# Kernel tuning notes

Hardware: AMD Instinct MI355X
Metric: run time of the kernel (lower is better)

## Reference

```python
import jax, jax.numpy as jnp
import numpy as np

B, T, D_IN, H, C = 4096, 20, 300, 512, 10


def setup_inputs() -> dict:
    key = jax.random.key(0)
    ks = jax.random.split(key, 12)
    s = lambda fan_in, fan_out: float(np.sqrt(6.0 / (fan_in + fan_out)))  # xavier uniform bound
    u = lambda k, shape, b: jax.random.uniform(k, shape, jnp.float32, -b, b)
    return {
        "x": jax.random.normal(ks[0], (B, T, D_IN), jnp.float32),
        "W_emb": u(ks[1], (D_IN, H), s(D_IN, H)),
        "b_emb": jnp.zeros((H,), jnp.float32),
        "wx0": u(ks[2], (H, H), s(H, H)),
        "wh0": u(ks[3], (H, H), s(H, H)),
        "b0": jnp.zeros((H,), jnp.float32),
        "wx1": u(ks[4], (H, H), s(H, H)),
        "wh1": u(ks[5], (H, H), s(H, H)),
        "b1": jnp.zeros((H,), jnp.float32),
        "wx2": u(ks[6], (H, H), s(H, H)),
        "wh2": u(ks[7], (H, H), s(H, H)),
        "b2": jnp.zeros((H,), jnp.float32),
        "W_fc": u(ks[8], (H, C), s(H, C)),
        "b_fc": jnp.zeros((C,), jnp.float32),
    }


def reference(x, W_emb, b_emb, wx0, wh0, b0, wx1, wh1, b1, wx2, wh2, b2, W_fc, b_fc):
    # embedding_layer applied to all timesteps: [B,T,300] -> [B,T,512]
    emb = jnp.einsum("btd,dh->bth", x, W_emb) + b_emb
    h0 = jnp.zeros((x.shape[0], wx0.shape[1]), x.dtype)
    init = (h0, h0, h0)

    def step(carry, v_t):  # v_t: [B,H]
        h0, h1, h2 = carry
        h0 = jnp.tanh(v_t @ wx0 + h0 @ wh0 + b0)
        h1 = jnp.tanh(h0 @ wx1 + h1 @ wh1 + b1)
        h2 = jnp.tanh(h1 @ wx2 + h2 @ wh2 + b2)
        return (h0, h1, h2), None

    (h0, h1, h2), _ = jax.lax.scan(step, init, jnp.swapaxes(emb, 0, 1))  # scan over T
    return h2 @ W_fc + b_fc  # [B, C]
```

## Files before the change

kernel.cpp:

```cpp
#include <hip/hip_runtime.h>

typedef _Float16 f16;
typedef _Float16 f16x8 __attribute__((ext_vector_type(8)));
typedef float floatx4 __attribute__((ext_vector_type(4)));

__device__ __forceinline__ float ftanh(float x) {
  float ax = __builtin_fabsf(x);
  float e  = __expf(-2.0f * ax);
  float t  = (1.0f - e) * __builtin_amdgcn_rcpf(1.0f + e);
  return x < 0.0f ? -t : t;
}

__device__ __forceinline__ void gll16(const f16* g, f16* l) {
  __builtin_amdgcn_global_load_lds(
      (const __attribute__((address_space(1))) void*)g,
      (__attribute__((address_space(3))) void*)l, 16, 0, 0);
}

template<int FJ>
__device__ __forceinline__ void tile_gemm(
    const f16* __restrict__ A0, int ldA0,
    const f16* __restrict__ A1, int ldA1,
    int K, const f16* __restrict__ WT,
    const float* __restrict__ bias,
    f16* __restrict__ outp, int bm, int bn, f16* sm)
{
  constexpr int TN = FJ * 32;
  constexpr int NJ = FJ;
  const int tid  = threadIdx.x;
  const int w    = tid >> 6;
  const int lane = tid & 63;
  const int lm   = lane & 15;
  const int quad = lane >> 4;
  const int wm   = (w >> 1) * 32;
  const int wn   = (w & 1) * (TN / 2);
  const int srow8 = lane >> 3;
  const int scol  = ((lane & 7) ^ srow8) * 8;
  const int lmx   = lane & 7;
  constexpr int SB = 8192 + TN * 64;

  floatx4 acc[2][NJ];
  #pragma unroll
  for (int i = 0; i < 2; ++i)
    #pragma unroll
    for (int j = 0; j < NJ; ++j)
      acc[i][j] = (floatx4){0.f, 0.f, 0.f, 0.f};

  auto stage = [&](int buf, int k0) {
    const f16* Asrc = (k0 < 512) ? (A0 + k0) : (A1 + (k0 - 512));
    const int  ld   = (k0 < 512) ? ldA0 : ldA1;
    f16* As0 = sm + buf * SB;
    f16* Ws0 = As0 + 8192;
    #pragma unroll
    for (int i = 0; i < 2; ++i) {
      int r = w * 16 + i * 8 + srow8;
      gll16(Asrc + (size_t)(bm + r) * ld + scol, As0 + (w * 2 + i) * 512);
    }
    #pragma unroll
    for (int i = 0; i < TN / 64; ++i) {
      int r = (w * (TN / 64) + i) * 8 + srow8;
      gll16(WT + (size_t)(bn + r) * K + k0 + scol, Ws0 + (w * (TN / 64) + i) * 512);
    }
  };

  const int NS = K >> 6;
  stage(0, 0);
  __syncthreads();
  for (int s = 0; s < NS; ++s) {
    if (s + 1 < NS) stage((s + 1) & 1, (s + 1) << 6);
    const f16* As0 = sm + (s & 1) * SB;
    const f16* Ws0 = As0 + 8192;
    #pragma unroll
    for (int kk = 0; kk < 64; kk += 32) {
      const int sw = (((kk >> 3) + quad) ^ lmx) << 3;
      f16x8 a[2], bfr[NJ];
      #pragma unroll
      for (int mi = 0; mi < 2; ++mi)
        a[mi] = *(const f16x8*)&As0[(size_t)(wm + mi * 16 + lm) * 64 + sw];
      #pragma unroll
      for (int nj = 0; nj < NJ; ++nj)
        bfr[nj] = *(const f16x8*)&Ws0[(size_t)(wn + nj * 16 + lm) * 64 + sw];
      #pragma unroll
      for (int mi = 0; mi < 2; ++mi)
        #pragma unroll
        for (int nj = 0; nj < NJ; ++nj)
          acc[mi][nj] = __builtin_amdgcn_mfma_f32_16x16x32_f16(a[mi], bfr[nj], acc[mi][nj], 0, 0, 0);
    }
    __syncthreads();
  }

  constexpr int ES = TN + 8;
  #pragma unroll
  for (int mi = 0; mi < 2; ++mi)
    #pragma unroll
    for (int nj = 0; nj < NJ; ++nj) {
      int col = wn + nj * 16 + lm;
      #pragma unroll
      for (int r = 0; r < 4; ++r) {
        int row = wm + mi * 16 + quad * 4 + r;
        sm[row * ES + col] = (f16)acc[mi][nj][r];
      }
    }
  __syncthreads();
  constexpr int TPR = TN / 8;
  constexpr int RPP = 512 / TPR;
  #pragma unroll
  for (int p = 0; p < 128 / RPP; ++p) {
    int row = p * RPP + tid / TPR;
    int c8  = (tid % TPR) * 8;
    f16x8 ve = *(const f16x8*)&sm[row * ES + c8];
    floatx4 bv0 = *(const floatx4*)&bias[bn + c8];
    floatx4 bv1 = *(const floatx4*)&bias[bn + c8 + 4];
    union { f16 e[8]; f16x8 v; } o;
    #pragma unroll
    for (int j = 0; j < 4; ++j) o.e[j]     = (f16)ftanh((float)ve[j]     + bv0[j]);
    #pragma unroll
    for (int j = 0; j < 4; ++j) o.e[4 + j] = (f16)ftanh((float)ve[4 + j] + bv1[j]);
    *(f16x8*)(outp + (size_t)(bm + row) * 512 + bn + c8) = o.v;
  }
}

__global__ __launch_bounds__(512, 4)
void rnn_step(int wv, const f16* __restrict__ xh,
              const f16* __restrict__ W0T, const f16* __restrict__ W1T,
              const f16* __restrict__ W2T,
              const float* __restrict__ bcomb, const float* __restrict__ b1,
              const float* __restrict__ b2,
              const f16* __restrict__ H0c, f16* __restrict__ H0n,
              const f16* __restrict__ H1c, f16* __restrict__ H1n,
              const f16* __restrict__ H2c, f16* __restrict__ H2n)
{
  __shared__ f16 sm[32768];
  const int b   = blockIdx.x;
  const int xcd = b & 7;
  const int r   = b >> 3;

  if (r < 32) {
    if (wv > 19) return;
    const int slab = xcd * 4 + (r & 3);
    const int bn   = (r >> 2) * 64;
    tile_gemm<2>(H0c, 512, xh + (size_t)wv * 320, 6400, 832, W0T, bcomb,
                 H0n, slab * 128, bn, sm);
  } else if (r < 48) {
    if (wv < 1 || wv > 20) return;
    const int rr   = r - 32;
    const int slab = xcd * 4 + (rr & 3);
    const int bn   = (rr >> 2) * 128;
    tile_gemm<4>(H0c, 512, H1c, 512, 1024, W1T, b1, H1n, slab * 128, bn, sm);
  } else {
    if (wv < 2) return;
    const int rr   = r - 48;
    const int slab = xcd * 4 + (rr & 3);
    const int bn   = (rr >> 2) * 128;
    tile_gemm<4>(H1c, 512, H2c, 512, 1024, W2T, b2, H2n, slab * 128, bn, sm);
  }
}

#define PX_N 1600

__global__ __launch_bounds__(256)
void prep_x(const float* __restrict__ x, f16* __restrict__ xh)
{
  const int NTH = PX_N * 256;
  const int g = blockIdx.x * 256 + threadIdx.x;
  floatx4 va[8], vb[8];
  int rw[8], cc[8];
  const floatx4 z4 = {0.f, 0.f, 0.f, 0.f};
  #pragma unroll
  for (int s = 0; s < 8; ++s) {
    int U = g + s * NTH;
    int row = U / 40;
    int c   = (U - row * 40) * 8;
    rw[s] = row; cc[s] = c;
    const float* src = x + (size_t)row * 300 + c;
    va[s] = (c + 4 <= 300) ? *(const floatx4*)src : z4;
    vb[s] = (c + 8 <= 300) ? *(const floatx4*)(src + 4) : z4;
  }
  #pragma unroll
  for (int s = 0; s < 8; ++s) {
    union { f16 e[8]; f16x8 v; } t;
    #pragma unroll
    for (int j = 0; j < 4; ++j) { t.e[j] = (f16)va[s][j]; t.e[4 + j] = (f16)vb[s][j]; }
    *(f16x8*)(xh + (size_t)rw[s] * 320 + cc[s]) = t.v;
  }
}

#define PW_WCE 2560
#define PW_BC  2568
#define PW_WT  3208
#define PW_Z   6280

__global__ __launch_bounds__(256)
void prep_w(const float* __restrict__ W_emb, const float* __restrict__ b_emb,
            const float* __restrict__ wx0, const float* __restrict__ wh0,
            const float* __restrict__ b0,
            const float* __restrict__ wx1, const float* __restrict__ wh1,
            const float* __restrict__ wx2, const float* __restrict__ wh2,
            f16* __restrict__ W0T, f16* __restrict__ W1T, f16* __restrict__ W2T,
            float* __restrict__ bcomb,
            f16* __restrict__ H0a, f16* __restrict__ H1b, f16* __restrict__ H2a)
{
  __shared__ float red[256];
  const int b   = blockIdx.x;
  const int tid = threadIdx.x;

  if (b < PW_WCE) {
    int oidx  = b * 64 + (tid & 63);
    int chunk = tid >> 6;
    int n = oidx & 511, k = oidx >> 9;
    float s = 0.f;
    if (k < 300) {
      const float* we = W_emb + k * 512 + chunk * 128;
      const float* wx = wx0 + (size_t)(chunk * 128) * 512 + n;
      #pragma unroll 4
      for (int j = 0; j < 128; ++j)
        s = __builtin_fmaf(we[j], wx[(size_t)j * 512], s);
    }
    red[tid] = s;
    __syncthreads();
    if (chunk == 0)
      W0T[(size_t)n * 832 + 512 + k] =
          (f16)(red[tid] + red[tid + 64] + red[tid + 128] + red[tid + 192]);
  } else if (b < PW_BC) {
    int n     = (b - PW_WCE) * 64 + (tid & 63);
    int chunk = tid >> 6;
    float s = 0.f;
    const float* be = b_emb + chunk * 128;
    const float* wx = wx0 + (size_t)(chunk * 128) * 512 + n;
    #pragma unroll 4
    for (int j = 0; j < 128; ++j)
      s = __builtin_fmaf(be[j], wx[(size_t)j * 512], s);
    red[tid] = s;
    __syncthreads();
    if (chunk == 0)
      bcomb[n] = b0[n] + red[tid] + red[tid + 64] + red[tid + 128] + red[tid + 192];
  } else if (b < PW_WT) {
    int id = (b - PW_BC) * 256 + tid;
    if (id < 32768) {
      int n = id & 511, k8 = id >> 9;
      union { f16 e[8]; f16x8 v; } t;
      #pragma unroll
      for (int j = 0; j < 8; ++j) t.e[j] = (f16)wh0[(size_t)(k8 * 8 + j) * 512 + n];
      *(f16x8*)&W0T[(size_t)n * 832 + k8 * 8] = t.v;
    } else if (id < 98304) {
      int i2 = id - 32768;
      int n = i2 & 511, k8 = i2 >> 9;
      union { f16 e[8]; f16x8 v; } t;
      const float* src = (k8 < 64) ? (wx1 + (size_t)(k8 * 8) * 512 + n)
                                   : (wh1 + (size_t)((k8 - 64) * 8) * 512 + n);
      #pragma unroll
      for (int j = 0; j < 8; ++j) t.e[j] = (f16)src[(size_t)j * 512];
      *(f16x8*)&W1T[(size_t)n * 1024 + k8 * 8] = t.v;
    } else {
      int i2 = id - 98304;
      int n = i2 & 511, k8 = i2 >> 9;
      union { f16 e[8]; f16x8 v; } t;
      const float* src = (k8 < 64) ? (wx2 + (size_t)(k8 * 8) * 512 + n)
                                   : (wh2 + (size_t)((k8 - 64) * 8) * 512 + n);
      #pragma unroll
      for (int j = 0; j < 8; ++j) t.e[j] = (f16)src[(size_t)j * 512];
      *(f16x8*)&W2T[(size_t)n * 1024 + k8 * 8] = t.v;
    }
  } else {
    int id = (b - PW_WT) * 256 + tid;
    f16x8 z8 = {};
    f16* dst = (id < 262144) ? H0a : (id < 524288) ? H1b : H2a;
    *(f16x8*)(dst + (size_t)(id & 262143) * 8) = z8;
  }
}

__global__ void fc_kernel(const f16* __restrict__ h2,
                          const float* __restrict__ Wfc, const float* __restrict__ bfc,
                          float* __restrict__ out)
{
  __shared__ float wf[5120];
  __shared__ float bf[16];
  const int tid = threadIdx.x;
  for (int i = tid; i < 5120; i += 256) wf[i] = Wfc[i];
  if (tid < 10) bf[tid] = bfc[tid];
  __syncthreads();
  int id = blockIdx.x * 256 + tid;
  int row = id / 10;
  int c = id - row * 10;
  float s = bf[c];
  const f16* hr = h2 + (size_t)row * 512;
  for (int k8 = 0; k8 < 64; ++k8) {
    f16x8 h8 = *(const f16x8*)(hr + k8 * 8);
    #pragma unroll
    for (int j = 0; j < 8; ++j)
      s = __builtin_fmaf((float)h8[j], wf[(k8 * 8 + j) * 10 + c], s);
  }
  out[id] = s;
}

extern "C" void kernel_launch(void* const* d_in, const int* in_sizes, int n_in,
                              void* d_out, int out_size, void* d_ws, size_t ws_size,
                              hipStream_t stream)
{
  (void)in_sizes; (void)n_in; (void)out_size; (void)ws_size;
  const float* x     = (const float*)d_in[0];
  const float* W_emb = (const float*)d_in[1];
  const float* b_emb = (const float*)d_in[2];
  const float* wx0   = (const float*)d_in[3];
  const float* wh0   = (const float*)d_in[4];
  const float* b0    = (const float*)d_in[5];
  const float* wx1   = (const float*)d_in[6];
  const float* wh1   = (const float*)d_in[7];
  const float* b1    = (const float*)d_in[8];
  const float* wx2   = (const float*)d_in[9];
  const float* wh2   = (const float*)d_in[10];
  const float* b2    = (const float*)d_in[11];
  const float* W_fc  = (const float*)d_in[12];
  const float* b_fc  = (const float*)d_in[13];
  float* out = (float*)d_out;

  char* ws = (char*)d_ws;
  size_t off = 0;
  auto alloc = [&](size_t bytes) -> void* {
    void* p = ws + off;
    off = (off + bytes + 255) & ~(size_t)255;
    return p;
  };
  f16*   xh    = (f16*)alloc((size_t)81920 * 320 * 2);
  f16*   W0T   = (f16*)alloc((size_t)512 * 832 * 2);
  f16*   W1T   = (f16*)alloc((size_t)512 * 1024 * 2);
  f16*   W2T   = (f16*)alloc((size_t)512 * 1024 * 2);
  float* bcomb = (float*)alloc(512 * 4);
  f16*   H0a   = (f16*)alloc((size_t)4096 * 512 * 2);
  f16*   H0b   = (f16*)alloc((size_t)4096 * 512 * 2);
  f16*   H1a   = (f16*)alloc((size_t)4096 * 512 * 2);
  f16*   H1b   = (f16*)alloc((size_t)4096 * 512 * 2);
  f16*   H2a   = (f16*)alloc((size_t)4096 * 512 * 2);
  f16*   H2b   = (f16*)alloc((size_t)4096 * 512 * 2);

  prep_x<<<PX_N, 256, 0, stream>>>(x, xh);
  prep_w<<<PW_Z, 256, 0, stream>>>(W_emb, b_emb, wx0, wh0, b0,
                                   wx1, wh1, wx2, wh2,
                                   W0T, W1T, W2T, bcomb, H0a, H1b, H2a);

  for (int wv = 0; wv < 22; ++wv) {
    const int cur = wv & 1;
    f16* H0c = cur ? H0b : H0a;  f16* H0n = cur ? H0a : H0b;
    f16* H1c = cur ? H1b : H1a;  f16* H1n = cur ? H1a : H1b;
    f16* H2c = cur ? H2b : H2a;  f16* H2n = cur ? H2a : H2b;
    rnn_step<<<512, 512, 0, stream>>>(wv, xh, W0T, W1T, W2T, bcomb, b1, b2,
                                      H0c, H0n, H1c, H1n, H2c, H2n);
  }

  fc_kernel<<<160, 256, 0, stream>>>(H2a, W_fc, b_fc, out);
}
```

Before: 596.0 us.

## Use 4-wave blocks with 128x64 tiles for all three RNN layers

Each workgroup drops from 8 waves to 4, and each wave now computes a 64x32 (or larger) register tile with 4 M-fragments instead of 2. All three layers use uniform 128x64 tiles, so layers 1 and 2 get twice as many blocks and the grid becomes 768 blocks of 256 threads. Shared memory per block shrinks, and the launch bounds change to 256 threads with 3 blocks per CU. The aim is more fragment reuse per LDS read and better load balance across layers, at the cost of higher register pressure per thread and fewer waves per block to hide latency.

```diff
diff --git a/kernel.cpp b/kernel.cpp
--- a/kernel.cpp
+++ b/kernel.cpp
@@ -25,25 +25,23 @@
     const float* __restrict__ bias,
     f16* __restrict__ outp, int bm, int bn, f16* sm)
 {
-  constexpr int TN = FJ * 32;
-  constexpr int NJ = FJ;
   const int tid  = threadIdx.x;
   const int w    = tid >> 6;
   const int lane = tid & 63;
   const int lm   = lane & 15;
   const int quad = lane >> 4;
-  const int wm   = (w >> 1) * 32;
-  const int wn   = (w & 1) * (TN / 2);
+  const int wm   = (w >> 1) * 64;
+  const int wn   = (w & 1) * (FJ * 16);
   const int srow8 = lane >> 3;
   const int scol  = ((lane & 7) ^ srow8) * 8;
   const int lmx   = lane & 7;
-  constexpr int SB = 8192 + TN * 64;
-
-  floatx4 acc[2][NJ];
-  #pragma unroll
-  for (int i = 0; i < 2; ++i)
-    #pragma unroll
-    for (int j = 0; j < NJ; ++j)
+  constexpr int SB = 8192 + FJ * 2048;
+
+  floatx4 acc[4][FJ];
+  #pragma unroll
+  for (int i = 0; i < 4; ++i)
+    #pragma unroll
+    for (int j = 0; j < FJ; ++j)
       acc[i][j] = (floatx4){0.f, 0.f, 0.f, 0.f};
 
   auto stage = [&](int buf, int k0) {
@@ -52,14 +50,14 @@
     f16* As0 = sm + buf * SB;
     f16* Ws0 = As0 + 8192;
     #pragma unroll
-    for (int i = 0; i < 2; ++i) {
-      int r = w * 16 + i * 8 + srow8;
-      gll16(Asrc + (size_t)(bm + r) * ld + scol, As0 + (w * 2 + i) * 512);
-    }
-    #pragma unroll
-    for (int i = 0; i < TN / 64; ++i) {
-      int r = (w * (TN / 64) + i) * 8 + srow8;
-      gll16(WT + (size_t)(bn + r) * K + k0 + scol, Ws0 + (w * (TN / 64) + i) * 512);
+    for (int i = 0; i < 4; ++i) {
+      int r = (w * 4 + i) * 8 + srow8;
+      gll16(Asrc + (size_t)(bm + r) * ld + scol, As0 + (w * 4 + i) * 512);
+    }
+    #pragma unroll
+    for (int i = 0; i < FJ; ++i) {
+      int r = (w * FJ + i) * 8 + srow8;
+      gll16(WT + (size_t)(bn + r) * K + k0 + scol, Ws0 + (w * FJ + i) * 512);
     }
   };
 
@@ -73,37 +71,37 @@
     #pragma unroll
     for (int kk = 0; kk < 64; kk += 32) {
       const int sw = (((kk >> 3) + quad) ^ lmx) << 3;
-      f16x8 a[2], bfr[NJ];
-      #pragma unroll
-      for (int mi = 0; mi < 2; ++mi)
-        a[mi] = *(const f16x8*)&As0[(size_t)(wm + mi * 16 + lm) * 64 + sw];
-      #pragma unroll
-      for (int nj = 0; nj < NJ; ++nj)
-        bfr[nj] = *(const f16x8*)&Ws0[(size_t)(wn + nj * 16 + lm) * 64 + sw];
-      #pragma unroll
-      for (int mi = 0; mi < 2; ++mi)
+      f16x8 a[4], bfr[FJ];
+      #pragma unroll
+      for (int fi = 0; fi < 4; ++fi)
+        a[fi] = *(const f16x8*)&As0[(size_t)(wm + fi * 16 + lm) * 64 + sw];
+      #pragma unroll
+      for (int fj = 0; fj < FJ; ++fj)
+        bfr[fj] = *(const f16x8*)&Ws0[(size_t)(wn + fj * 16 + lm) * 64 + sw];
+      #pragma unroll
+      for (int fi = 0; fi < 4; ++fi)
         #pragma unroll
-        for (int nj = 0; nj < NJ; ++nj)
-          acc[mi][nj] = __builtin_amdgcn_mfma_f32_16x16x32_f16(a[mi], bfr[nj], acc[mi][nj], 0, 0, 0);
+        for (int fj = 0; fj < FJ; ++fj)
+          acc[fi][fj] = __builtin_amdgcn_mfma_f32_16x16x32_f16(a[fi], bfr[fj], acc[fi][fj], 0, 0, 0);
     }
     __syncthreads();
   }
 
-  constexpr int ES = TN + 8;
-  #pragma unroll
-  for (int mi = 0; mi < 2; ++mi)
-    #pragma unroll
-    for (int nj = 0; nj < NJ; ++nj) {
-      int col = wn + nj * 16 + lm;
+  constexpr int ES = FJ * 32 + 8;
+  #pragma unroll
+  for (int fi = 0; fi < 4; ++fi)
+    #pragma unroll
+    for (int fj = 0; fj < FJ; ++fj) {
+      int col = wn + fj * 16 + lm;
       #pragma unroll
       for (int r = 0; r < 4; ++r) {
-        int row = wm + mi * 16 + quad * 4 + r;
-        sm[row * ES + col] = (f16)acc[mi][nj][r];
+        int row = wm + fi * 16 + quad * 4 + r;
+        sm[row * ES + col] = (f16)acc[fi][fj][r];
       }
     }
   __syncthreads();
-  constexpr int TPR = TN / 8;
-  constexpr int RPP = 512 / TPR;
+  constexpr int TPR = (FJ * 32) / 8;
+  constexpr int RPP = 256 / TPR;
   #pragma unroll
   for (int p = 0; p < 128 / RPP; ++p) {
     int row = p * RPP + tid / TPR;
@@ -120,7 +118,7 @@
   }
 }
 
-__global__ __launch_bounds__(512, 4)
+__global__ __launch_bounds__(256, 3)
 void rnn_step(int wv, const f16* __restrict__ xh,
               const f16* __restrict__ W0T, const f16* __restrict__ W1T,
               const f16* __restrict__ W2T,
@@ -130,29 +128,23 @@
               const f16* __restrict__ H1c, f16* __restrict__ H1n,
               const f16* __restrict__ H2c, f16* __restrict__ H2n)
 {
-  __shared__ f16 sm[32768];
+  __shared__ f16 sm[24576];
   const int b   = blockIdx.x;
   const int xcd = b & 7;
   const int r   = b >> 3;
+  const int slab = xcd * 4 + (r & 3);
+  const int bn   = ((r >> 2) & 7) * 64;
 
   if (r < 32) {
     if (wv > 19) return;
-    const int slab = xcd * 4 + (r & 3);
-    const int bn   = (r >> 2) * 64;
     tile_gemm<2>(H0c, 512, xh + (size_t)wv * 320, 6400, 832, W0T, bcomb,
                  H0n, slab * 128, bn, sm);
-  } else if (r < 48) {
+  } else if (r < 64) {
     if (wv < 1 || wv > 20) return;
-    const int rr   = r - 32;
-    const int slab = xcd * 4 + (rr & 3);
-    const int bn   = (rr >> 2) * 128;
-    tile_gemm<4>(H0c, 512, H1c, 512, 1024, W1T, b1, H1n, slab * 128, bn, sm);
+    tile_gemm<2>(H0c, 512, H1c, 512, 1024, W1T, b1, H1n, slab * 128, bn, sm);
   } else {
     if (wv < 2) return;
-    const int rr   = r - 48;
-    const int slab = xcd * 4 + (rr & 3);
-    const int bn   = (rr >> 2) * 128;
-    tile_gemm<4>(H1c, 512, H2c, 512, 1024, W2T, b2, H2n, slab * 128, bn, sm);
+    tile_gemm<2>(H1c, 512, H2c, 512, 1024, W2T, b2, H2n, slab * 128, bn, sm);
   }
 }
 
@@ -343,7 +335,7 @@
     f16* H0c = cur ? H0b : H0a;  f16* H0n = cur ? H0a : H0b;
     f16* H1c = cur ? H1b : H1a;  f16* H1n = cur ? H1a : H1b;
     f16* H2c = cur ? H2b : H2a;  f16* H2n = cur ? H2a : H2b;
-    rnn_step<<<512, 512, 0, stream>>>(wv, xh, W0T, W1T, W2T, bcomb, b1, b2,
+    rnn_step<<<768, 256, 0, stream>>>(wv, xh, W0T, W1T, W2T, bcomb, b1, b2,
                                       H0c, H0n, H1c, H1n, H2c, H2n);
   }
 
```

New measurement: 626.6 us. 1.05x slower.
